# Optimization experiments

Hardware: AMD Instinct MI355X
Metric: run time of the kernel (lower is better)

Reference implementation:

```python
import jax, jax.numpy as jnp
import numpy as np

# Config matching init_kwargs: in_dim=128, kernal_sz=8 -> d=16 units per side
D = 16      # grid of units per side
K = 8       # kernel (patch) size
C = 3       # input channels
OUT = 1000  # out_chnls (codebook size per unit)
B = 64      # batch
BETA = 10.0 # softmax temperature (init arg beta)


def setup_inputs() -> dict:
    key = jax.random.key(0)
    k1, k2 = jax.random.split(key)
    x = jax.random.normal(k1, (B, C, D * K, D * K), dtype=jnp.float32)
    # Independent weights per (w,h) unit: [d, d, out_chnls, k*k*C]
    W = jax.random.normal(k2, (D, D, OUT, C * K * K), dtype=jnp.float32) * 0.02
    return {"x": x, "W": W}


def reference(x, W):
    Bn = x.shape[0]
    P = C * K * K
    # Patch extraction matching x[:, :, k*w:k*w+k, k*h:k*h+k].reshape(B, -1)
    # (channel-major flatten of each non-overlapping k x k patch)
    patches = (
        x.reshape(Bn, C, D, K, D, K)          # (b, c, w, kh, h, kw)
         .transpose(0, 2, 4, 1, 3, 5)          # (b, w, h, c, kh, kw)
         .reshape(Bn, D, D, P)
    )
    # infer: per-unit linear infer_step -> a[b, o, w, h]
    a = jnp.einsum('bwhp,whop->bowh', patches, W)
    # per-patch competitive softmax selection over the unit's channels
    z = jax.nn.softmax(BETA * a, axis=1)
    # predict: decode code back to patch via W^T, scatter back into image
    pred = jnp.einsum('bowh,whop->bwhp', z, W)
    p = (
        pred.reshape(Bn, D, D, C, K, K)        # (b, w, h, c, kh, kw)
            .transpose(0, 3, 1, 4, 2, 5)        # (b, c, w, kh, h, kw)
            .reshape(Bn, C, D * K, D * K)
    )
    return p
```

## Files before the change

### kernel.cpp

```cpp
#include <hip/hip_runtime.h>


#define Dd 16
#define OUTC 1000
#define Pp 192
#define Bb 64
#define OT 64
#define NT 16
#define THREADS 1024
#define BETA 10.0f

typedef __attribute__((ext_vector_type(8))) short short8;
typedef __attribute__((ext_vector_type(4))) float f32x4;

#define MFMA(a, b, c) __builtin_amdgcn_mfma_f32_16x16x32_bf16((a), (b), (c), 0, 0, 0)

__device__ __forceinline__ unsigned f2bf(float f) {
  unsigned u = __float_as_uint(f);
  return (u + 0x7fffu + ((u >> 16) & 1u)) >> 16;
}

__device__ __forceinline__ int paddr(int b, int p) {
  return b * 384 + ((((p) >> 3) ^ (b & 7)) << 4) + ((p) & 7) * 2;
}
__device__ __forceinline__ int waddr(int o, int p) {
  int f = (o & 7) ^ ((o >> 3) & 3);
  return o * 384 + ((((p) >> 3) ^ f) << 4) + ((p) & 7) * 2;
}
__device__ __forceinline__ int eaddr(int b, int o) {
  return b * 128 + ((((o) >> 3) ^ (b & 7)) << 4) + ((o) & 7) * 2;
}

__device__ __forceinline__ void cvt_hilo4(const float4 v, uint2& hi2, uint2& lo2) {
  unsigned h0 = f2bf(v.x), h1 = f2bf(v.y), h2 = f2bf(v.z), h3 = f2bf(v.w);
  float l0 = v.x - __uint_as_float(h0 << 16);
  float l1 = v.y - __uint_as_float(h1 << 16);
  float l2 = v.z - __uint_as_float(h2 << 16);
  float l3 = v.w - __uint_as_float(h3 << 16);
  unsigned g0 = f2bf(l0), g1 = f2bf(l1), g2 = f2bf(l2), g3 = f2bf(l3);
  hi2 = make_uint2(h0 | (h1 << 16), h2 | (h3 << 16));
  lo2 = make_uint2(g0 | (g1 << 16), g2 | (g3 << 16));
}

__global__ __launch_bounds__(THREADS, 4)
void local_layer_mfma2(const float* __restrict__ x,
                       const float* __restrict__ W,
                       float* __restrict__ out) {
  __shared__ unsigned short pH[Bb * Pp];
  __shared__ unsigned short pL[Bb * Pp];
  __shared__ unsigned short wH2[2][OT * Pp];
  __shared__ unsigned short wL2[2][OT * Pp];
  __shared__ unsigned short eSs[Bb * OT];
  __shared__ float lS[Bb];

  char* pHc = (char*)pH; char* pLc = (char*)pL;
  char* eSc = (char*)eSs;

  const int u = blockIdx.x, uw = u >> 4, uh = u & 15;
  const int tid = threadIdx.x;
  const int wv = tid >> 6, lane = tid & 63;
  const int lr = lane & 15, lg = lane >> 4;
  const int mq = wv & 3;
  const int ow = wv >> 2;
  const int bB = 16 * mq;

  const float* Wu = W + (size_t)u * (OUTC * Pp);

  if (tid < Bb) lS[tid] = 0.f;

  float4 R[3];
#pragma unroll
  for (int k = 0; k < 3; ++k) {
    int i4 = tid + THREADS * k;
    int o = i4 / 48, p = (i4 % 48) * 4;
    R[k] = *reinterpret_cast<const float4*>(Wu + o * Pp + p);
  }

#pragma unroll
  for (int k = 0; k < 3; ++k) {
    int i4 = tid + THREADS * k;
    int b = i4 / 48, q = i4 % 48, p = q * 4;
    int c = p >> 6, kh = (p >> 3) & 7, kw = p & 7;
    float4 v = *reinterpret_cast<const float4*>(
        x + ((size_t)((b * 3 + c) * 128 + uw * 8 + kh) * 128 + uh * 8 + kw));
    uint2 hi2, lo2;
    cvt_hilo4(v, hi2, lo2);
    *reinterpret_cast<uint2*>(pHc + paddr(b, p)) = hi2;
    *reinterpret_cast<uint2*>(pLc + paddr(b, p)) = lo2;
  }

  {
    char* wHc = (char*)wH2[0];
    char* wLc = (char*)wL2[0];
#pragma unroll
    for (int k = 0; k < 3; ++k) {
      int i4 = tid + THREADS * k;
      int o = i4 / 48, p = (i4 % 48) * 4;
      uint2 hi2, lo2;
      cvt_hilo4(R[k], hi2, lo2);
      *reinterpret_cast<uint2*>(wHc + waddr(o, p)) = hi2;
      *reinterpret_cast<uint2*>(wLc + waddr(o, p)) = lo2;
    }
  }
  __syncthreads();

  short8 pa_h[6];
#pragma unroll
  for (int ks = 0; ks < 6; ++ks)
    pa_h[ks] = *reinterpret_cast<const short8*>(pHc + paddr(bB + lr, 32 * ks + 8 * lg));

  f32x4 pacc[3];
#pragma unroll
  for (int f = 0; f < 3; ++f) pacc[f] = (f32x4){0.f, 0.f, 0.f, 0.f};
  float lPart[4] = {0.f, 0.f, 0.f, 0.f};

  for (int t = 0; t < NT; ++t) {
    char* wHc = (char*)wH2[t & 1];
    char* wLc = (char*)wL2[t & 1];

    if (t + 1 < NT) {
#pragma unroll
      for (int k = 0; k < 3; ++k) {
        int i4 = tid + THREADS * k;
        int o = i4 / 48, p = (i4 % 48) * 4;
        int o_g = (t + 1) * OT + o;
        R[k] = (o_g < OUTC)
                   ? *reinterpret_cast<const float4*>(Wu + (size_t)o_g * Pp + p)
                   : make_float4(0.f, 0.f, 0.f, 0.f);
      }
    }

    f32x4 acc = (f32x4){0.f, 0.f, 0.f, 0.f};
#pragma unroll
    for (int ks = 0; ks < 6; ++ks) {
      const int ko = 32 * ks + 8 * lg;
      short8 wbh = *reinterpret_cast<const short8*>(wHc + waddr(16 * ow + lr, ko));
      short8 wbl = *reinterpret_cast<const short8*>(wLc + waddr(16 * ow + lr, ko));
      short8 pal = *reinterpret_cast<const short8*>(pLc + paddr(bB + lr, ko));
      acc = MFMA(pa_h[ks], wbh, acc);
      acc = MFMA(pa_h[ks], wbl, acc);
      acc = MFMA(pal, wbh, acc);
    }

    {
      const int o_g = t * OT + 16 * ow + lr;
      const bool valid = (o_g < OUTC);
#pragma unroll
      for (int j = 0; j < 4; ++j) {
        float e = valid ? __expf(BETA * acc[j]) : 0.f;
        lPart[j] += e;
        *reinterpret_cast<unsigned short*>(
            eSc + eaddr(bB + 4 * lg + j, 16 * ow + lr)) = (unsigned short)f2bf(e);
      }
    }
    __syncthreads();

    short8 ea[2];
#pragma unroll
    for (int ks2 = 0; ks2 < 2; ++ks2)
      ea[ks2] = *reinterpret_cast<const short8*>(
          eSc + eaddr(bB + lr, 32 * ks2 + 8 * lg));

#pragma unroll
    for (int f = 0; f < 3; ++f) {
      const int p = 48 * ow + 16 * f + lr;
#pragma unroll
      for (int ks2 = 0; ks2 < 2; ++ks2) {
        short8 wb;
#pragma unroll
        for (int e8 = 0; e8 < 8; ++e8)
          wb[e8] = *reinterpret_cast<const short*>(
              wHc + waddr(32 * ks2 + 8 * lg + e8, p));
        pacc[f] = MFMA(ea[ks2], wb, pacc[f]);
      }
    }

    if (t + 1 < NT) {
      char* nH = (char*)wH2[(t + 1) & 1];
      char* nL = (char*)wL2[(t + 1) & 1];
#pragma unroll
      for (int k = 0; k < 3; ++k) {
        int i4 = tid + THREADS * k;
        int o = i4 / 48, p = (i4 % 48) * 4;
        uint2 hi2, lo2;
        cvt_hilo4(R[k], hi2, lo2);
        *reinterpret_cast<uint2*>(nH + waddr(o, p)) = hi2;
        *reinterpret_cast<uint2*>(nL + waddr(o, p)) = lo2;
      }
    }
    __syncthreads();
  }

#pragma unroll
  for (int j = 0; j < 4; ++j) {
    float v = lPart[j];
    v += __shfl_xor(v, 1, 16);
    v += __shfl_xor(v, 2, 16);
    v += __shfl_xor(v, 4, 16);
    v += __shfl_xor(v, 8, 16);
    if (lr == 0) atomicAdd(&lS[bB + 4 * lg + j], v);
  }
  __syncthreads();

  float inv[4];
#pragma unroll
  for (int j = 0; j < 4; ++j) inv[j] = 1.f / lS[bB + 4 * lg + j];
#pragma unroll
  for (int f = 0; f < 3; ++f) {
    const int p = 48 * ow + 16 * f + lr;
    const int c = p >> 6, kh = (p >> 3) & 7, kw = p & 7;
#pragma unroll
    for (int j = 0; j < 4; ++j) {
      const int b = bB + 4 * lg + j;
      out[((size_t)((b * 3 + c) * 128 + uw * 8 + kh)) * 128 + uh * 8 + kw] =
          pacc[f][j] * inv[j];
    }
  }
}

extern "C" void kernel_launch(void* const* d_in, const int* in_sizes, int n_in,
                              void* d_out, int out_size, void* d_ws, size_t ws_size,
                              hipStream_t stream) {
  const float* x = (const float*)d_in[0];
  const float* W = (const float*)d_in[1];
  float* out = (float*)d_out;
  hipLaunchKernelGGL(local_layer_mfma2, dim3(Dd * Dd), dim3(THREADS), 0, stream,
                     x, W, out);
}
```

Before: 310.7 us.

## Split output channels across two blocks per unit and drop W low-part MFMAs

After: 320.5 us. +3.1%, slower.

```diff
diff --git a/kernel.cpp b/kernel.cpp
--- a/kernel.cpp
+++ b/kernel.cpp
@@ -1,13 +1,12 @@
 #include <hip/hip_runtime.h>
 
 
-#define Dd 16
 #define OUTC 1000
 #define Pp 192
 #define Bb 64
-#define OT 64
+#define OT 32
 #define NT 16
-#define THREADS 1024
+#define THREADS 512
 #define BETA 10.0f
 
 typedef __attribute__((ext_vector_type(8))) short short8;
@@ -28,164 +27,135 @@
   return o * 384 + ((((p) >> 3) ^ f) << 4) + ((p) & 7) * 2;
 }
 __device__ __forceinline__ int eaddr(int b, int o) {
-  return b * 128 + ((((o) >> 3) ^ (b & 7)) << 4) + ((o) & 7) * 2;
-}
-
-__device__ __forceinline__ void cvt_hilo4(const float4 v, uint2& hi2, uint2& lo2) {
-  unsigned h0 = f2bf(v.x), h1 = f2bf(v.y), h2 = f2bf(v.z), h3 = f2bf(v.w);
-  float l0 = v.x - __uint_as_float(h0 << 16);
-  float l1 = v.y - __uint_as_float(h1 << 16);
-  float l2 = v.z - __uint_as_float(h2 << 16);
-  float l3 = v.w - __uint_as_float(h3 << 16);
-  unsigned g0 = f2bf(l0), g1 = f2bf(l1), g2 = f2bf(l2), g3 = f2bf(l3);
-  hi2 = make_uint2(h0 | (h1 << 16), h2 | (h3 << 16));
-  lo2 = make_uint2(g0 | (g1 << 16), g2 | (g3 << 16));
+  return b * 80 + o * 2;
 }
 
 __global__ __launch_bounds__(THREADS, 4)
-void local_layer_mfma2(const float* __restrict__ x,
-                       const float* __restrict__ W,
-                       float* __restrict__ out) {
+void ll_main(const float* __restrict__ x, const float* __restrict__ W,
+             float* __restrict__ predWs, float* __restrict__ lWs) {
   __shared__ unsigned short pH[Bb * Pp];
   __shared__ unsigned short pL[Bb * Pp];
-  __shared__ unsigned short wH2[2][OT * Pp];
-  __shared__ unsigned short wL2[2][OT * Pp];
-  __shared__ unsigned short eSs[Bb * OT];
-  __shared__ float lS[Bb];
-
-  char* pHc = (char*)pH; char* pLc = (char*)pL;
-  char* eSc = (char*)eSs;
-
-  const int u = blockIdx.x, uw = u >> 4, uh = u & 15;
-  const int tid = threadIdx.x;
-  const int wv = tid >> 6, lane = tid & 63;
+  __shared__ unsigned short wHb[2][OT * Pp];
+  __shared__ unsigned short eSs[Bb * 40];
+  char* pHc = (char*)pH; char* pLc = (char*)pL; char* eSc = (char*)eSs;
+
+  const int bid = blockIdx.x;
+  const int u = bid >> 1, q = bid & 1;
+  const int uw = u >> 4, uh = u & 15;
+  const int obase = q * 512;
+  const int tid = threadIdx.x, wv = tid >> 6, lane = tid & 63;
   const int lr = lane & 15, lg = lane >> 4;
-  const int mq = wv & 3;
-  const int ow = wv >> 2;
-  const int bB = 16 * mq;
+  const int mq = wv & 3, ov = wv >> 2;
+  const int mw = wv & 1, ow = wv >> 1;
 
   const float* Wu = W + (size_t)u * (OUTC * Pp);
 
-  if (tid < Bb) lS[tid] = 0.f;
+#pragma unroll
+  for (int k = 0; k < 6; ++k) {
+    int i4 = tid + THREADS * k;
+    int b = i4 / 48, p = (i4 % 48) * 4;
+    int c = p >> 6, kh = (p >> 3) & 7, kw = p & 7;
+    float4 v = *reinterpret_cast<const float4*>(
+        x + ((size_t)((b * 3 + c) * 128 + uw * 8 + kh) * 128 + uh * 8 + kw));
+    unsigned h0 = f2bf(v.x), h1 = f2bf(v.y), h2 = f2bf(v.z), h3 = f2bf(v.w);
+    float l0 = v.x - __uint_as_float(h0 << 16);
+    float l1 = v.y - __uint_as_float(h1 << 16);
+    float l2 = v.z - __uint_as_float(h2 << 16);
+    float l3 = v.w - __uint_as_float(h3 << 16);
+    unsigned g0 = f2bf(l0), g1 = f2bf(l1), g2 = f2bf(l2), g3 = f2bf(l3);
+    *reinterpret_cast<uint2*>(pHc + paddr(b, p)) = make_uint2(h0 | (h1 << 16), h2 | (h3 << 16));
+    *reinterpret_cast<uint2*>(pLc + paddr(b, p)) = make_uint2(g0 | (g1 << 16), g2 | (g3 << 16));
+  }
 
   float4 R[3];
 #pragma unroll
   for (int k = 0; k < 3; ++k) {
     int i4 = tid + THREADS * k;
     int o = i4 / 48, p = (i4 % 48) * 4;
-    R[k] = *reinterpret_cast<const float4*>(Wu + o * Pp + p);
-  }
-
+    int og = obase + o; og = og < OUTC ? og : OUTC - 1;
+    R[k] = *reinterpret_cast<const float4*>(Wu + (size_t)og * Pp + p);
+  }
 #pragma unroll
   for (int k = 0; k < 3; ++k) {
     int i4 = tid + THREADS * k;
-    int b = i4 / 48, q = i4 % 48, p = q * 4;
-    int c = p >> 6, kh = (p >> 3) & 7, kw = p & 7;
-    float4 v = *reinterpret_cast<const float4*>(
-        x + ((size_t)((b * 3 + c) * 128 + uw * 8 + kh) * 128 + uh * 8 + kw));
-    uint2 hi2, lo2;
-    cvt_hilo4(v, hi2, lo2);
-    *reinterpret_cast<uint2*>(pHc + paddr(b, p)) = hi2;
-    *reinterpret_cast<uint2*>(pLc + paddr(b, p)) = lo2;
-  }
-
-  {
-    char* wHc = (char*)wH2[0];
-    char* wLc = (char*)wL2[0];
-#pragma unroll
-    for (int k = 0; k < 3; ++k) {
-      int i4 = tid + THREADS * k;
-      int o = i4 / 48, p = (i4 % 48) * 4;
-      uint2 hi2, lo2;
-      cvt_hilo4(R[k], hi2, lo2);
-      *reinterpret_cast<uint2*>(wHc + waddr(o, p)) = hi2;
-      *reinterpret_cast<uint2*>(wLc + waddr(o, p)) = lo2;
-    }
+    int o = i4 / 48, p = (i4 % 48) * 4;
+    unsigned h0 = f2bf(R[k].x), h1 = f2bf(R[k].y), h2 = f2bf(R[k].z), h3 = f2bf(R[k].w);
+    *reinterpret_cast<uint2*>((char*)wHb[0] + waddr(o, p)) =
+        make_uint2(h0 | (h1 << 16), h2 | (h3 << 16));
   }
   __syncthreads();
 
   short8 pa_h[6];
 #pragma unroll
   for (int ks = 0; ks < 6; ++ks)
-    pa_h[ks] = *reinterpret_cast<const short8*>(pHc + paddr(bB + lr, 32 * ks + 8 * lg));
-
-  f32x4 pacc[3];
-#pragma unroll
-  for (int f = 0; f < 3; ++f) pacc[f] = (f32x4){0.f, 0.f, 0.f, 0.f};
+    pa_h[ks] = *reinterpret_cast<const short8*>(pHc + paddr(16 * mq + lr, 32 * ks + 8 * lg));
+
+  f32x4 pacc[2][3];
+#pragma unroll
+  for (int h = 0; h < 2; ++h)
+#pragma unroll
+    for (int f = 0; f < 3; ++f) pacc[h][f] = (f32x4){0.f, 0.f, 0.f, 0.f};
   float lPart[4] = {0.f, 0.f, 0.f, 0.f};
 
   for (int t = 0; t < NT; ++t) {
-    char* wHc = (char*)wH2[t & 1];
-    char* wLc = (char*)wL2[t & 1];
+    char* wc = (char*)wHb[t & 1];
 
     if (t + 1 < NT) {
 #pragma unroll
       for (int k = 0; k < 3; ++k) {
         int i4 = tid + THREADS * k;
         int o = i4 / 48, p = (i4 % 48) * 4;
-        int o_g = (t + 1) * OT + o;
-        R[k] = (o_g < OUTC)
-                   ? *reinterpret_cast<const float4*>(Wu + (size_t)o_g * Pp + p)
-                   : make_float4(0.f, 0.f, 0.f, 0.f);
+        int og = obase + (t + 1) * OT + o; og = og < OUTC ? og : OUTC - 1;
+        R[k] = *reinterpret_cast<const float4*>(Wu + (size_t)og * Pp + p);
       }
     }
 
-    f32x4 acc = (f32x4){0.f, 0.f, 0.f, 0.f};
+    f32x4 aH = (f32x4){0.f, 0.f, 0.f, 0.f};
+    f32x4 aL = (f32x4){0.f, 0.f, 0.f, 0.f};
 #pragma unroll
     for (int ks = 0; ks < 6; ++ks) {
       const int ko = 32 * ks + 8 * lg;
-      short8 wbh = *reinterpret_cast<const short8*>(wHc + waddr(16 * ow + lr, ko));
-      short8 wbl = *reinterpret_cast<const short8*>(wLc + waddr(16 * ow + lr, ko));
-      short8 pal = *reinterpret_cast<const short8*>(pLc + paddr(bB + lr, ko));
-      acc = MFMA(pa_h[ks], wbh, acc);
-      acc = MFMA(pa_h[ks], wbl, acc);
-      acc = MFMA(pal, wbh, acc);
+      short8 wb = *reinterpret_cast<const short8*>(wc + waddr(16 * ov + lr, ko));
+      short8 pl = *reinterpret_cast<const short8*>(pLc + paddr(16 * mq + lr, ko));
+      aH = MFMA(pa_h[ks], wb, aH);
+      aL = MFMA(pl, wb, aL);
     }
 
     {
-      const int o_g = t * OT + 16 * ow + lr;
-      const bool valid = (o_g < OUTC);
+      const int o_l = 16 * ov + lr;
+      const bool valid = (obase + t * OT + o_l) < OUTC;
 #pragma unroll
       for (int j = 0; j < 4; ++j) {
-        float e = valid ? __expf(BETA * acc[j]) : 0.f;
+        float e = valid ? __expf(BETA * (aH[j] + aL[j])) : 0.f;
         lPart[j] += e;
         *reinterpret_cast<unsigned short*>(
-            eSc + eaddr(bB + 4 * lg + j, 16 * ow + lr)) = (unsigned short)f2bf(e);
+            eSc + eaddr(16 * mq + 4 * lg + j, o_l)) = (unsigned short)f2bf(e);
       }
     }
     __syncthreads();
 
-    short8 ea[2];
-#pragma unroll
-    for (int ks2 = 0; ks2 < 2; ++ks2)
-      ea[ks2] = *reinterpret_cast<const short8*>(
-          eSc + eaddr(bB + lr, 32 * ks2 + 8 * lg));
-
+    short8 ea0 = *reinterpret_cast<const short8*>(eSc + eaddr(32 * mw + lr, 8 * lg));
+    short8 ea1 = *reinterpret_cast<const short8*>(eSc + eaddr(32 * mw + 16 + lr, 8 * lg));
 #pragma unroll
     for (int f = 0; f < 3; ++f) {
       const int p = 48 * ow + 16 * f + lr;
-#pragma unroll
-      for (int ks2 = 0; ks2 < 2; ++ks2) {
-        short8 wb;
-#pragma unroll
-        for (int e8 = 0; e8 < 8; ++e8)
-          wb[e8] = *reinterpret_cast<const short*>(
-              wHc + waddr(32 * ks2 + 8 * lg + e8, p));
-        pacc[f] = MFMA(ea[ks2], wb, pacc[f]);
-      }
+      short8 wb;
+#pragma unroll
+      for (int e8 = 0; e8 < 8; ++e8)
+        wb[e8] = *reinterpret_cast<const short*>(wc + waddr(8 * lg + e8, p));
+      pacc[0][f] = MFMA(ea0, wb, pacc[0][f]);
+      pacc[1][f] = MFMA(ea1, wb, pacc[1][f]);
     }
 
     if (t + 1 < NT) {
-      char* nH = (char*)wH2[(t + 1) & 1];
-      char* nL = (char*)wL2[(t + 1) & 1];
+      char* nc = (char*)wHb[(t + 1) & 1];
 #pragma unroll
       for (int k = 0; k < 3; ++k) {
         int i4 = tid + THREADS * k;
         int o = i4 / 48, p = (i4 % 48) * 4;
-        uint2 hi2, lo2;
-        cvt_hilo4(R[k], hi2, lo2);
-        *reinterpret_cast<uint2*>(nH + waddr(o, p)) = hi2;
-        *reinterpret_cast<uint2*>(nL + waddr(o, p)) = lo2;
+        unsigned h0 = f2bf(R[k].x), h1 = f2bf(R[k].y), h2 = f2bf(R[k].z), h3 = f2bf(R[k].w);
+        *reinterpret_cast<uint2*>(nc + waddr(o, p)) =
+            make_uint2(h0 | (h1 << 16), h2 | (h3 << 16));
       }
     }
     __syncthreads();
@@ -198,24 +168,39 @@
     v += __shfl_xor(v, 2, 16);
     v += __shfl_xor(v, 4, 16);
     v += __shfl_xor(v, 8, 16);
-    if (lr == 0) atomicAdd(&lS[bB + 4 * lg + j], v);
-  }
-  __syncthreads();
-
-  float inv[4];
-#pragma unroll
-  for (int j = 0; j < 4; ++j) inv[j] = 1.f / lS[bB + 4 * lg + j];
-#pragma unroll
-  for (int f = 0; f < 3; ++f) {
-    const int p = 48 * ow + 16 * f + lr;
-    const int c = p >> 6, kh = (p >> 3) & 7, kw = p & 7;
-#pragma unroll
-    for (int j = 0; j < 4; ++j) {
-      const int b = bB + 4 * lg + j;
-      out[((size_t)((b * 3 + c) * 128 + uw * 8 + kh)) * 128 + uh * 8 + kw] =
-          pacc[f][j] * inv[j];
-    }
-  }
+    if (lr == 0)
+      lWs[(u * 2 + q) * 128 + ov * 64 + 16 * mq + 4 * lg + j] = v;
+  }
+
+  float* P = predWs + (size_t)(u * 2 + q) * (Bb * Pp);
+#pragma unroll
+  for (int h = 0; h < 2; ++h)
+#pragma unroll
+    for (int f = 0; f < 3; ++f) {
+      const int p = 48 * ow + 16 * f + lr;
+#pragma unroll
+      for (int j = 0; j < 4; ++j)
+        P[(32 * mw + 16 * h + 4 * lg + j) * Pp + p] = pacc[h][f][j];
+    }
+}
+
+__global__ __launch_bounds__(256)
+void ll_fin(const float* __restrict__ predWs, const float* __restrict__ lWs,
+            float* __restrict__ out) {
+  int t4 = blockIdx.x * 256 + threadIdx.x;
+  int f = t4 * 4;
+  int Y = f & 127, X = (f >> 7) & 127, r = f >> 14;
+  int c = r % 3, b = r / 3;
+  int uw = X >> 3, kh = X & 7, uh = Y >> 3, kw = Y & 7;
+  int u = uw * 16 + uh, p = c * 64 + kh * 8 + kw;
+  float4 s0 = *reinterpret_cast<const float4*>(predWs + (size_t)(2 * u) * (Bb * Pp) + b * Pp + p);
+  float4 s1 = *reinterpret_cast<const float4*>(predWs + (size_t)(2 * u + 1) * (Bb * Pp) + b * Pp + p);
+  float l = lWs[(2 * u) * 128 + b] + lWs[(2 * u) * 128 + 64 + b] +
+            lWs[(2 * u + 1) * 128 + b] + lWs[(2 * u + 1) * 128 + 64 + b];
+  float inv = 1.f / l;
+  float4 o4 = make_float4((s0.x + s1.x) * inv, (s0.y + s1.y) * inv,
+                          (s0.z + s1.z) * inv, (s0.w + s1.w) * inv);
+  *reinterpret_cast<float4*>(out + f) = o4;
 }
 
 extern "C" void kernel_launch(void* const* d_in, const int* in_sizes, int n_in,
@@ -224,6 +209,8 @@
   const float* x = (const float*)d_in[0];
   const float* W = (const float*)d_in[1];
   float* out = (float*)d_out;
-  hipLaunchKernelGGL(local_layer_mfma2, dim3(Dd * Dd), dim3(THREADS), 0, stream,
-                     x, W, out);
-}
+  float* predWs = (float*)d_ws;
+  float* lWs = predWs + (size_t)512 * (Bb * Pp);
+  hipLaunchKernelGGL(ll_main, dim3(512), dim3(THREADS), 0, stream, x, W, predWs, lWs);
+  hipLaunchKernelGGL(ll_fin, dim3(3072), dim3(256), 0, stream, predWs, lWs, out);
+}
```
